# Kernel tuning notes

Measured on AMD Instinct MI355X. Metric: run time of the kernel, lower is better.

## Reference

```python
import jax, jax.numpy as jnp
import numpy as np

N = 6            # ensemble members (must match share_mode '6-1')
IN_C = 128
OUT_C = 128
K = 3
STRIDE = 1
PAD = 1
D = IN_C * OUT_C * K * K  # 147456
TEMP = 1.0
ZP1 = 1.2
ZP2 = -0.2
RES_DENOS = (3.0, 5.0)   # res_denos[:maxBWPow] with bw=2 -> [2**2-1, 2**2+1]


def round_ste(v):
    # straight-through round: forward round, backward identity
    return v + jax.lax.stop_gradient(jnp.round(v) - v)


def setup_inputs() -> dict:
    key = jax.random.key(0)
    k1, k2, k3, k4 = jax.random.split(key, 4)
    x = jax.random.normal(k1, (48, IN_C, 64, 64), jnp.float32)
    U = jax.random.normal(k2, (N, D), jnp.float32)
    bp = jax.random.normal(k3, (N + 1, D), jnp.float32)
    # uniform noise for the gumbel-sigmoid sample (open interval to avoid log(0))
    u = jax.random.uniform(k4, (N + 1, D), jnp.float32, 1e-6, 1.0 - 1e-6)
    return {"x": x, "U": U, "bp": bp, "u": u}


def reference(x, U, bp, u):
    beta = jnp.max(U)
    alpha = jnp.min(U)

    # gumbel-sigmoid gating
    g = jnp.log(u / (1.0 - u))
    bsamples = jax.nn.sigmoid((g + bp) / TEMP)
    gates = jnp.clip(bsamples * (ZP1 - ZP2) + ZP2, 0.0, 1.0)  # (7, D)
    # first 6 rows: per-member gates for level 0; last row shared across members for level 1
    gates = jnp.stack([gates[:N], jnp.broadcast_to(gates[N:], (N, D))], axis=0)  # (2, N, D)
    order_gates = jax.lax.stop_gradient(
        jnp.cumprod((gates > 0).astype(gates.dtype), axis=0)
    )

    # sequential residual-bit STE quantization (2 levels)
    s1 = (beta - alpha) / RES_DENOS[0]
    v1 = s1 * round_ste(U / s1)                       # (N, D)
    s2 = s1 / RES_DENOS[1]
    v2 = s2 * round_ste((U - v1.mean(0)) / s2)        # (N, D); vals.sum(0).mean(0) == v1.mean(0)
    vals = jnp.stack([v1, v2], axis=0)                # (2, N, D)

    w = (vals * (gates * order_gates)).sum(0)         # (N, D)
    w = w.reshape(OUT_C * N, IN_C, K, K)

    B = x.shape[0]
    xr = x.reshape(B // N, N * x.shape[1], x.shape[2], x.shape[3])
    act = jax.lax.conv_general_dilated(
        xr, w,
        window_strides=(STRIDE, STRIDE),
        padding=[(PAD, PAD), (PAD, PAD)],
        dimension_numbers=('NCHW', 'OIHW', 'NCHW'),
        feature_group_count=N,
    )
    return act.reshape(act.shape[0] * N, act.shape[1] // N, act.shape[2], act.shape[3])
```

## Files before the change

kernel.cpp:

```cpp
#include <hip/hip_runtime.h>
#include <stdint.h>

typedef __attribute__((ext_vector_type(8))) short bf16x8;
typedef __attribute__((ext_vector_type(4))) float f32x4;

#define DW 147456
#define NTOT (6 * DW)

__device__ __forceinline__ unsigned short f2bf(float f) {
    unsigned int u = __float_as_uint(f);
    u = (u + 0x7FFFu + ((u >> 16) & 1u)) >> 16;
    return (unsigned short)u;
}

__global__ __launch_bounds__(256) void reduce_part(const float* __restrict__ U,
                                                   float* __restrict__ part) {
    int tid = threadIdx.x;
    float mx = -INFINITY, mn = INFINITY;
    const float4* U4 = (const float4*)U;
    for (int i = blockIdx.x * 256 + tid; i < NTOT / 4; i += 256 * 256) {
        float4 v = U4[i];
        mx = fmaxf(fmaxf(fmaxf(mx, v.x), v.y), fmaxf(v.z, v.w));
        mn = fminf(fminf(fminf(mn, v.x), v.y), fminf(v.z, v.w));
    }
    __shared__ float smx[256], smn[256];
    smx[tid] = mx; smn[tid] = mn;
    __syncthreads();
    for (int s = 128; s > 0; s >>= 1) {
        if (tid < s) {
            smx[tid] = fmaxf(smx[tid], smx[tid + s]);
            smn[tid] = fminf(smn[tid], smn[tid + s]);
        }
        __syncthreads();
    }
    if (tid == 0) { part[blockIdx.x] = smx[0]; part[256 + blockIdx.x] = smn[0]; }
}

__global__ __launch_bounds__(256) void make_weights(const float* __restrict__ U,
                                                    const float* __restrict__ bp,
                                                    const float* __restrict__ uu,
                                                    const float* __restrict__ part,
                                                    unsigned short* __restrict__ Wb2) {
    int tid = threadIdx.x;
    __shared__ float smx[256], smn[256];
    smx[tid] = part[tid]; smn[tid] = part[256 + tid];
    __syncthreads();
    for (int s = 128; s > 0; s >>= 1) {
        if (tid < s) {
            smx[tid] = fmaxf(smx[tid], smx[tid + s]);
            smn[tid] = fminf(smn[tid], smn[tid + s]);
        }
        __syncthreads();
    }
    float beta = smx[0], alpha = smn[0];
    float s1 = (beta - alpha) / 3.0f;
    float s2 = s1 / 5.0f;

    int d = blockIdx.x * 256 + tid;

    float v1[6]; float Uv[6]; float vsum = 0.f;
    #pragma unroll
    for (int n = 0; n < 6; n++) {
        float Un = U[n * DW + d];
        Uv[n] = Un;
        float v = s1 * rintf(Un / s1);
        v1[n] = v; vsum += v;
    }
    float vmean = vsum / 6.0f;

    float g6;
    {
        float un = uu[6 * DW + d];
        float sg = un / (un + (1.0f - un) * expf(-bp[6 * DW + d]));
        g6 = fminf(fmaxf(sg * 1.4f - 0.2f, 0.0f), 1.0f);
    }

    int oc = d / 1152;
    int rem = d - oc * 1152;
    int ic = rem / 9;
    int t9 = rem - ic * 9;
    int c = ic >> 5, icc = ic & 31;
    int och = oc >> 6, ocl = oc & 63;
    int mi = ocl >> 4, lrr = ocl & 15;
    int lq = icc >> 3, jj = icc & 7;
    size_t base = ((size_t)(c * 2 + och) * 9 + t9) * 2048
                + (size_t)mi * 512 + (size_t)(lq * 16 + lrr) * 8 + jj;

    #pragma unroll
    for (int n = 0; n < 6; n++) {
        float un = uu[n * DW + d];
        float sg = un / (un + (1.0f - un) * expf(-bp[n * DW + d]));
        float g0 = fminf(fmaxf(sg * 1.4f - 0.2f, 0.0f), 1.0f);
        float v2 = s2 * rintf((Uv[n] - vmean) / s2);
        float w = v1[n] * g0 + ((g0 > 0.0f && g6 > 0.0f) ? v2 * g6 : 0.0f);
        Wb2[(size_t)n * DW + base] = f2bf(w);
    }
}

__global__ __launch_bounds__(256) void transform_x(const float* __restrict__ x,
                                                   unsigned short* __restrict__ xT) {
    __shared__ unsigned short Sh[128 * 70];
    int b = blockIdx.x;
    int img = b >> 6, row = b & 63;
    int tid = threadIdx.x;
    {
        int ch = tid >> 1;
        int col0 = (tid & 1) * 32;
        const float* src = x + (((size_t)(img * 128 + ch) * 64 + row) * 64 + col0);
        #pragma unroll
        for (int j = 0; j < 8; j++) {
            float4 v = ((const float4*)src)[j];
            unsigned int p0 = (unsigned int)f2bf(v.x) | ((unsigned int)f2bf(v.y) << 16);
            unsigned int p1 = (unsigned int)f2bf(v.z) | ((unsigned int)f2bf(v.w) << 16);
            unsigned int* dst = (unsigned int*)&Sh[ch * 70 + col0 + j * 4];
            dst[0] = p0; dst[1] = p1;
        }
    }
    __syncthreads();
    {
        int col = tid & 63;
        int q = tid >> 6;
        int chg = q * 32;
        int h = ((col + 1) >> 1) & 3;
        union { unsigned short s[32]; uint4 v[4]; } tmp;
        #pragma unroll
        for (int j = 0; j < 32; j++) tmp.s[j] = Sh[(chg + j) * 70 + col];
        uint4 a = tmp.v[0], bb = tmp.v[1], c2 = tmp.v[2], d2 = tmp.v[3];
        if (h & 1) { uint4 t = a; a = bb; bb = t; t = c2; c2 = d2; d2 = t; }
        if (h & 2) { uint4 t = a; a = c2; c2 = t; t = bb; bb = d2; d2 = t; }
        uint4* dst = (uint4*)(xT + ((size_t)img * 524288 + (size_t)q * 131072 +
                                    (size_t)row * 2048 + col * 32));
        dst[0] = a; dst[1] = bb; dst[2] = c2; dst[3] = d2;
    }
}

typedef const __attribute__((address_space(1))) void CGV;
typedef __attribute__((address_space(3))) void LV;

__global__ __launch_bounds__(256, 2) void conv_mfma(const unsigned short* __restrict__ xT,
                                                    const unsigned short* __restrict__ Wb2,
                                                    float* __restrict__ out) {
    __shared__ __align__(16) unsigned short Xs[6 * 66 * 32];
    __shared__ __align__(16) unsigned short Ws[9 * 64 * 32];
    int o = blockIdx.x;
    int blk = (o & 7) * 192 + (o >> 3);
    int band = blk & 15;
    int och = (blk >> 4) & 1;
    int img = blk >> 5;
    int row0 = band * 4;
    int mem = img - (img / 6) * 6;
    const unsigned short* Wmem = Wb2 + (size_t)mem * DW;
    const unsigned short* Xsrc = xT + (size_t)img * 524288;

    int tid = threadIdx.x;
    int lane = tid & 63;
    int prow = tid >> 6;
    int lr = lane & 15, lq = lane >> 4;
    int so0 = (lq ^ ((lr >> 1) & 3)) * 8;
    int so1 = (lq ^ (((lr + 1) >> 1) & 3)) * 8;
    int so2 = (lq ^ (((lr + 2) >> 1) & 3)) * 8;

    if (tid < 192) {
        int r = tid >> 5, j = tid & 31;
        int col = (j < 16) ? 0 : 65;
        *(unsigned int*)&Xs[(r * 66 + col) * 32 + (j & 15) * 2] = 0u;
    }

    auto stage = [&](int c) {
        const unsigned short* wsrc = Wmem + (size_t)((c * 2 + och) * 9) * 2048;
        #pragma unroll
        for (int t = 0; t < 9; t++)
            __builtin_amdgcn_global_load_lds((CGV*)(wsrc + t * 2048 + tid * 8),
                                             (LV*)(&Ws[t * 2048 + tid * 8]), 16, 0, 0);
        #pragma unroll
        for (int r = 0; r < 6; r++) {
            int srow = row0 + r - 1;
            if ((unsigned)srow < 64u)
                __builtin_amdgcn_global_load_lds((CGV*)(Xsrc + c * 131072 + srow * 2048 + tid * 8),
                                                 (LV*)(&Xs[(r * 66 + 1) * 32 + tid * 8]), 16, 0, 0);
            else
                *(uint4*)&Xs[(r * 66 + 1) * 32 + tid * 8] = make_uint4(0u, 0u, 0u, 0u);
        }
    };

    f32x4 acc[4][4];
    #pragma unroll
    for (int mi = 0; mi < 4; mi++)
        #pragma unroll
        for (int ni = 0; ni < 4; ni++)
            acc[mi][ni] = (f32x4){0.f, 0.f, 0.f, 0.f};

    stage(0);
    __syncthreads();

    for (int c = 0; c < 4; c++) {
        #pragma unroll
        for (int t = 0; t < 9; t++) {
            const int dy = t / 3, dx = t - (t / 3) * 3;
            const int so = (dx == 0) ? so0 : (dx == 1) ? so1 : so2;
            bf16x8 af[4], bfr[4];
            #pragma unroll
            for (int mi = 0; mi < 4; mi++)
                af[mi] = *(const bf16x8*)(&Ws[t * 2048 + mi * 512 + lane * 8]);
            #pragma unroll
            for (int ni = 0; ni < 4; ni++) {
                int col = ni * 16 + lr + dx;
                bfr[ni] = *(const bf16x8*)(&Xs[((prow + dy) * 66 + col) * 32 + so]);
            }
            #pragma unroll
            for (int mi = 0; mi < 4; mi++)
                #pragma unroll
                for (int ni = 0; ni < 4; ni++)
                    acc[mi][ni] = __builtin_amdgcn_mfma_f32_16x16x32_bf16(
                        af[mi], bfr[ni], acc[mi][ni], 0, 0, 0);
        }
        if (c < 3) {
            __syncthreads();
            stage(c + 1);
            __syncthreads();
        }
    }

    float* obase = out + (size_t)img * 524288 + (size_t)(row0 + prow) * 64;
    #pragma unroll
    for (int mi = 0; mi < 4; mi++) {
        #pragma unroll
        for (int ni = 0; ni < 4; ni++) {
            int px = ni * 16 + lr;
            int ocb = och * 64 + mi * 16 + lq * 4;
            #pragma unroll
            for (int rr = 0; rr < 4; rr++)
                obase[(size_t)(ocb + rr) * 4096 + px] = acc[mi][ni][rr];
        }
    }
}

extern "C" void kernel_launch(void* const* d_in, const int* in_sizes, int n_in,
                              void* d_out, int out_size, void* d_ws, size_t ws_size,
                              hipStream_t stream) {
    const float* x  = (const float*)d_in[0];
    const float* U  = (const float*)d_in[1];
    const float* bp = (const float*)d_in[2];
    const float* uu = (const float*)d_in[3];
    float* out = (float*)d_out;

    char* ws = (char*)d_ws;
    float* part = (float*)ws;
    unsigned short* Wb2 = (unsigned short*)(ws + 4096);
    unsigned short* xT  = (unsigned short*)(ws + 4096 + 1769472);

    reduce_part <<<256, 256, 0, stream>>>(U, part);
    make_weights<<<576, 256, 0, stream>>>(U, bp, uu, part, Wb2);
    transform_x <<<48 * 64, 256, 0, stream>>>(x, xT);
    conv_mfma   <<<48 * 32, 256, 0, stream>>>(xT, Wb2, out);
}
```

Baseline: 251.3 us.

## Double-buffer LDS stages in conv MFMA kernel to overlap loads with compute

```diff
diff --git a/kernel.cpp b/kernel.cpp
--- a/kernel.cpp
+++ b/kernel.cpp
@@ -137,11 +137,14 @@
 typedef const __attribute__((address_space(1))) void CGV;
 typedef __attribute__((address_space(3))) void LV;
 
-__global__ __launch_bounds__(256, 2) void conv_mfma(const unsigned short* __restrict__ xT,
+#define XSZ (6 * 66 * 32)
+#define WSZ (9 * 64 * 32)
+
+__global__ __launch_bounds__(256, 1) void conv_mfma(const unsigned short* __restrict__ xT,
                                                     const unsigned short* __restrict__ Wb2,
                                                     float* __restrict__ out) {
-    __shared__ __align__(16) unsigned short Xs[6 * 66 * 32];
-    __shared__ __align__(16) unsigned short Ws[9 * 64 * 32];
+    __shared__ __align__(16) unsigned short Xs[2 * XSZ];
+    __shared__ __align__(16) unsigned short Ws[2 * WSZ];
     int o = blockIdx.x;
     int blk = (o & 7) * 192 + (o >> 3);
     int band = blk & 15;
@@ -164,22 +167,25 @@
         int r = tid >> 5, j = tid & 31;
         int col = (j < 16) ? 0 : 65;
         *(unsigned int*)&Xs[(r * 66 + col) * 32 + (j & 15) * 2] = 0u;
-    }
-
-    auto stage = [&](int c) {
+        *(unsigned int*)&Xs[XSZ + (r * 66 + col) * 32 + (j & 15) * 2] = 0u;
+    }
+
+    auto stage = [&](int c, int p) {
         const unsigned short* wsrc = Wmem + (size_t)((c * 2 + och) * 9) * 2048;
+        unsigned short* Wp = &Ws[p * WSZ];
+        unsigned short* Xp = &Xs[p * XSZ];
         #pragma unroll
         for (int t = 0; t < 9; t++)
             __builtin_amdgcn_global_load_lds((CGV*)(wsrc + t * 2048 + tid * 8),
-                                             (LV*)(&Ws[t * 2048 + tid * 8]), 16, 0, 0);
+                                             (LV*)(&Wp[t * 2048 + tid * 8]), 16, 0, 0);
         #pragma unroll
         for (int r = 0; r < 6; r++) {
             int srow = row0 + r - 1;
             if ((unsigned)srow < 64u)
                 __builtin_amdgcn_global_load_lds((CGV*)(Xsrc + c * 131072 + srow * 2048 + tid * 8),
-                                                 (LV*)(&Xs[(r * 66 + 1) * 32 + tid * 8]), 16, 0, 0);
+                                                 (LV*)(&Xp[(r * 66 + 1) * 32 + tid * 8]), 16, 0, 0);
             else
-                *(uint4*)&Xs[(r * 66 + 1) * 32 + tid * 8] = make_uint4(0u, 0u, 0u, 0u);
+                *(uint4*)&Xp[(r * 66 + 1) * 32 + tid * 8] = make_uint4(0u, 0u, 0u, 0u);
         }
     };
 
@@ -190,10 +196,14 @@
         for (int ni = 0; ni < 4; ni++)
             acc[mi][ni] = (f32x4){0.f, 0.f, 0.f, 0.f};
 
-    stage(0);
+    stage(0, 0);
     __syncthreads();
 
     for (int c = 0; c < 4; c++) {
+        int cur = c & 1;
+        if (c < 3) stage(c + 1, cur ^ 1);
+        const unsigned short* Wc = &Ws[cur * WSZ];
+        const unsigned short* Xc = &Xs[cur * XSZ];
         #pragma unroll
         for (int t = 0; t < 9; t++) {
             const int dy = t / 3, dx = t - (t / 3) * 3;
@@ -201,11 +211,11 @@
             bf16x8 af[4], bfr[4];
             #pragma unroll
             for (int mi = 0; mi < 4; mi++)
-                af[mi] = *(const bf16x8*)(&Ws[t * 2048 + mi * 512 + lane * 8]);
+                af[mi] = *(const bf16x8*)(&Wc[t * 2048 + mi * 512 + lane * 8]);
             #pragma unroll
             for (int ni = 0; ni < 4; ni++) {
                 int col = ni * 16 + lr + dx;
-                bfr[ni] = *(const bf16x8*)(&Xs[((prow + dy) * 66 + col) * 32 + so]);
+                bfr[ni] = *(const bf16x8*)(&Xc[((prow + dy) * 66 + col) * 32 + so]);
             }
             #pragma unroll
             for (int mi = 0; mi < 4; mi++)
@@ -214,11 +224,8 @@
                     acc[mi][ni] = __builtin_amdgcn_mfma_f32_16x16x32_bf16(
                         af[mi], bfr[ni], acc[mi][ni], 0, 0, 0);
         }
-        if (c < 3) {
+        if (c < 3)
             __syncthreads();
-            stage(c + 1);
-            __syncthreads();
-        }
     }
 
     float* obase = out + (size_t)img * 524288 + (size_t)(row0 + prow) * 64;
```

New measurement: 264.9 us. 1.05x slower.
